# Optimization experiments

Hardware: AMD Instinct MI355X
Metric: run time of the kernel (lower is better)

Reference implementation:

```python
import jax, jax.numpy as jnp
import numpy as np

B, T, ENC, DEC, OUT = 512, 128, 256, 256, 1
Tm1 = T - 1


def setup_inputs() -> dict:
    key = jax.random.key(0)
    ks = jax.random.split(key, 14)
    s = lambda k, shape, scale=0.05: (jax.random.normal(k, shape, dtype=jnp.float32) * scale)
    return {
        "input_encoded": jax.random.normal(ks[0], (B, Tm1, ENC), dtype=jnp.float32),
        "y_history": jax.random.normal(ks[1], (B, Tm1, OUT), dtype=jnp.float32),
        # attn_layer: Linear(2*DEC+ENC -> ENC), Tanh, Linear(ENC -> 1)
        "W_attn1": s(ks[2], (ENC, 2 * DEC + ENC)),
        "b_attn1": s(ks[3], (ENC,)),
        "W_attn2": s(ks[4], (1, ENC)),
        "b_attn2": s(ks[5], (1,)),
        # single-layer LSTM cell (input_size=OUT, hidden=DEC); gate order i,f,g,o
        "W_ih": s(ks[6], (4 * DEC, OUT)),
        "W_hh": s(ks[7], (4 * DEC, DEC)),
        "b_ih": s(ks[8], (4 * DEC,)),
        "b_hh": s(ks[9], (4 * DEC,)),
        # fc: Linear(ENC+OUT -> OUT); torch code re-inits weight ~ N(0,1)
        "W_fc": jax.random.normal(ks[10], (OUT, ENC + OUT), dtype=jnp.float32),
        "b_fc": s(ks[11], (OUT,)),
        # fc_final: Linear(DEC+ENC -> OUT)
        "W_fcf": s(ks[12], (OUT, DEC + ENC)),
        "b_fcf": s(ks[13], (OUT,)),
    }


def reference(input_encoded, y_history, W_attn1, b_attn1, W_attn2, b_attn2,
              W_ih, W_hh, b_ih, b_hh, W_fc, b_fc, W_fcf, b_fcf):
    Bsz, tm1, enc = input_encoded.shape
    dec = W_hh.shape[1]
    h0 = jnp.zeros((Bsz, dec), dtype=input_encoded.dtype)
    c0 = jnp.zeros_like(h0)
    ctx0 = jnp.zeros((Bsz, enc), dtype=input_encoded.dtype)

    def step(carry, y_t):
        h, c, _ = carry  # h, c: [B, DEC]; y_t: [B, OUT]
        hs = jnp.broadcast_to(h[:, None, :], (Bsz, tm1, dec))
        cs = jnp.broadcast_to(c[:, None, :], (Bsz, tm1, dec))
        x = jnp.concatenate([hs, cs, input_encoded], axis=-1)  # [B, Tm1, 2*DEC+ENC]
        score = jnp.tanh(x @ W_attn1.T + b_attn1) @ W_attn2.T + b_attn2  # [B, Tm1, 1]
        attn = jax.nn.softmax(score[..., 0], axis=1)  # [B, Tm1]
        context = jnp.einsum('bt,bte->be', attn, input_encoded)  # [B, ENC]
        y_tilde = jnp.concatenate([context, y_t], axis=1) @ W_fc.T + b_fc  # [B, OUT]
        gates = y_tilde @ W_ih.T + b_ih + h @ W_hh.T + b_hh  # [B, 4*DEC]
        i, f, g, o = jnp.split(gates, 4, axis=1)
        c_new = jax.nn.sigmoid(f) * c + jax.nn.sigmoid(i) * jnp.tanh(g)
        h_new = jax.nn.sigmoid(o) * jnp.tanh(c_new)
        return (h_new, c_new, context), attn

    (h, c, context), attn_rows = jax.lax.scan(
        step, (h0, c0, ctx0), jnp.swapaxes(y_history, 0, 1))
    weight = jnp.swapaxes(attn_rows, 0, 1)  # [B, Tm1, Tm1]
    out = jnp.concatenate([h, context], axis=1) @ W_fcf.T + b_fcf  # [B, OUT]
    return out, weight
```

## Files before the change

kernel.cpp:

```cpp
#include <hip/hip_runtime.h>

typedef _Float16 f16;
typedef _Float16 h2 __attribute__((ext_vector_type(2)));
typedef _Float16 h4 __attribute__((ext_vector_type(4)));
typedef _Float16 h8 __attribute__((ext_vector_type(8)));

#define T127 127

__device__ __forceinline__ float rcp_f(float x) { return __builtin_amdgcn_rcpf(x); }

__device__ __forceinline__ float fdot2(h2 a, h2 b, float c) {
  return __builtin_amdgcn_fdot2(a, b, c, false);
}
__device__ __forceinline__ h2 mk2(f16 a, f16 b) { h2 v; v[0] = a; v[1] = b; return v; }

__device__ __forceinline__ float fast_tanh(float x) {
  x = fminf(fmaxf(x, -12.f), 12.f);
  float e = __expf(2.f * x);
  return (e - 1.f) * rcp_f(e + 1.f);
}
__device__ __forceinline__ float fast_sig(float x) {
  x = fminf(fmaxf(x, -30.f), 30.f);
  return rcp_f(1.f + __expf(-x));
}

__global__ void pack_wa1c(const float* __restrict__ Wa1, f16* __restrict__ wsA) {
  int tid = blockIdx.x * 256 + threadIdx.x;
  int it = tid >> 9, L = tid & 511;
  int k = L >> 1, g2 = L & 1;
  const float* src = Wa1 + (size_t)k * 768 + 256 + g2 * 128 + it * 8;
  f16* dst = wsA + (size_t)tid * 8;
#pragma unroll
  for (int j = 0; j < 8; ++j) dst[j] = (f16)src[j];
}

__global__ void pack_whh2(const float* __restrict__ Whh, f16* __restrict__ wsH) {
  int tid = blockIdx.x * 256 + threadIdx.x;
  int m = tid >> 9, L = tid & 511;
  int row = L + (m & 1) * 512;
  int it = m >> 1;
  const float* src = Whh + (size_t)row * 256 + it * 8;
  f16* dst = wsH + (size_t)tid * 8;
#pragma unroll
  for (int j = 0; j < 8; ++j) dst[j] = (f16)src[j];
}

__global__ __attribute__((amdgpu_flat_work_group_size(512, 512)))
void decoder_kernel(
    const float* __restrict__ enc,
    const float* __restrict__ yhist,
    const float* __restrict__ Wa1,
    const float* __restrict__ ba1,
    const float* __restrict__ Wa2,
    const float* __restrict__ ba2,
    const float* __restrict__ Wih,
    const float* __restrict__ bih,
    const float* __restrict__ bhh,
    const float* __restrict__ Wfc,
    const float* __restrict__ bfc,
    const float* __restrict__ Wfcf,
    const float* __restrict__ bfcf,
    const f16* __restrict__ wsA,
    const f16* __restrict__ wsH,
    float* __restrict__ outp)
{
  __shared__ __align__(16) f16 tE1[2][T127][272];
  __shared__ __align__(16) f16 hch[2][4][136];
  __shared__ __align__(16) float s_arr[2][4][68];
  __shared__ __align__(16) float score_s[2][128];
  __shared__ __align__(16) float p_s[2][128];
  __shared__ __align__(16) float q_s[2][128];
  __shared__ __align__(16) char ovl[8192];
  __shared__ __align__(16) float w2_lds[256];
  __shared__ __align__(16) float yh_s[2][128];
  __shared__ float ytil[2], ctxq_s[2], red[8];

  float* gact = (float*)ovl;
  f16* est = (f16*)ovl;

  const int L = threadIdx.x;
  const int b0 = blockIdx.x * 2;
  const int kL = L >> 1;
  const int g2 = L & 1;

  for (int i = L; i < 1088; i += 512) ((f16*)hch)[i] = (f16)0.f;
  if (L < 256) {
    w2_lds[L] = Wa2[L];
    int bb = L >> 7, tt = L & 127;
    if (tt < T127) yh_s[bb][tt] = yhist[(size_t)(b0 + bb) * T127 + tt];
  }
  float c_reg = 0.f;

  {
    h2 we1[64];
    {
      const float4* wrow = (const float4*)(Wa1 + (size_t)kL * 768 + 512 + g2 * 128);
#pragma unroll
      for (int i = 0; i < 32; ++i) {
        float4 w = wrow[i];
        we1[2 * i]     = mk2((f16)w.x, (f16)w.y);
        we1[2 * i + 1] = mk2((f16)w.z, (f16)w.w);
      }
    }
    const int prow = L >> 6;
    const int lm = L & 63;
    const int sg = lm >> 4;
    const int si = (lm * 4) & 63;

#pragma unroll 1
    for (int tt = 0; tt < 32; ++tt) {
      __syncthreads();
      {
        int bbs = prow >> 2, j4 = prow & 3, j = tt * 4 + j4;
        float4 v = make_float4(0.f, 0.f, 0.f, 0.f);
        if (j < T127)
          v = *(const float4*)(enc + (((size_t)(b0 + bbs)) * T127 + j) * 256 + lm * 4);
        h4 hv; hv[0] = (f16)v.x; hv[1] = (f16)v.y; hv[2] = (f16)v.z; hv[3] = (f16)v.w;
        *(h4*)(est + prow * 288 + sg * 72 + si) = hv;
      }
      __syncthreads();
#pragma unroll 1
      for (int P = 0; P < 8; ++P) {
        int bbs = P >> 2, j4 = P & 3, j = tt * 4 + j4;
        const h8* ep = (const h8*)(est + P * 288 + (2 * g2) * 72);
        const h8* ep2 = (const h8*)(est + P * 288 + (2 * g2 + 1) * 72);
        float a0 = 0.f, a1 = 0.f;
#pragma unroll
        for (int r = 0; r < 8; ++r) {
          h8 e8 = ep[r];
          a0 = fdot2(we1[4 * r + 0], mk2(e8[0], e8[1]), a0);
          a1 = fdot2(we1[4 * r + 1], mk2(e8[2], e8[3]), a1);
          a0 = fdot2(we1[4 * r + 2], mk2(e8[4], e8[5]), a0);
          a1 = fdot2(we1[4 * r + 3], mk2(e8[6], e8[7]), a1);
        }
#pragma unroll
        for (int r = 0; r < 8; ++r) {
          h8 e8 = ep2[r];
          a0 = fdot2(we1[32 + 4 * r + 0], mk2(e8[0], e8[1]), a0);
          a1 = fdot2(we1[32 + 4 * r + 1], mk2(e8[2], e8[3]), a1);
          a0 = fdot2(we1[32 + 4 * r + 2], mk2(e8[4], e8[5]), a0);
          a1 = fdot2(we1[32 + 4 * r + 3], mk2(e8[6], e8[7]), a1);
        }
        float acc = a0 + a1;
        acc += __shfl_xor(acc, 1, 64);
        if (g2 == 0 && j < T127)
          tE1[bbs][j][(kL >> 6) * 68 + (kL & 63)] = (f16)fast_tanh(acc);
      }
      {
        int bbs = prow >> 2, j4 = prow & 3, j = tt * 4 + j4;
        float4 wp4 = *(const float4*)(Wfc + lm * 4);
        float4 wq4 = *(const float4*)(Wfcf + 256 + lm * 4);
        h4 ev = *(const h4*)(est + prow * 288 + sg * 72 + si);
        float pacc = (float)ev[0] * wp4.x + (float)ev[1] * wp4.y + (float)ev[2] * wp4.z + (float)ev[3] * wp4.w;
        float qacc = (float)ev[0] * wq4.x + (float)ev[1] * wq4.y + (float)ev[2] * wq4.z + (float)ev[3] * wq4.w;
#pragma unroll
        for (int s = 32; s; s >>= 1) {
          pacc += __shfl_xor(pacc, s, 64);
          qacc += __shfl_xor(qacc, s, 64);
        }
        if (lm == 0 && j < T127) { p_s[bbs][j] = pacc; q_s[bbs][j] = qacc; }
      }
    }
  }
  __syncthreads();

  h2 w1h[64];
  {
    const float4* wrow = (const float4*)(Wa1 + (size_t)kL * 768 + g2 * 128);
#pragma unroll
    for (int i = 0; i < 32; ++i) {
      float4 w = wrow[i];
      w1h[2 * i]     = mk2((f16)w.x, (f16)w.y);
      w1h[2 * i + 1] = mk2((f16)w.z, (f16)w.w);
    }
  }
  const float b1k = ba1[kL];
  const float wihA = Wih[L];
  const float wihB = Wih[512 + L];
  const float biasA = bih[L] + bhh[L];
  const float biasB = bih[512 + L] + bhh[512 + L];
  const float ba2v = ba2[0];
  const float wfcy = Wfc[256];
  const float bfc0 = bfc[0];
  const int g_u = L & 3;
  __syncthreads();

#pragma unroll 1
  for (int t = 0; t < T127; ++t) {
    const h8* wA = (const h8*)wsA + L;
    const h8* wH = (const h8*)wsH + L;
    h8 a0 = wA[0], a1 = wA[512];
    h8 p0 = wH[0], p1 = wH[512], p2 = wH[1024], p3 = wH[1536];

    float u0a = 0.f, u0b = 0.f, u1a = 0.f, u1b = 0.f;
    {
      const h8* hp0 = (const h8*)&hch[0][g2][0];
      const h8* hp1 = (const h8*)&hch[1][g2][0];
#pragma unroll
      for (int r = 0; r < 16; ++r) {
        h8 x = hp0[r];
        u0a = fdot2(w1h[4 * r + 0], mk2(x[0], x[1]), u0a);
        u0b = fdot2(w1h[4 * r + 1], mk2(x[2], x[3]), u0b);
        u0a = fdot2(w1h[4 * r + 2], mk2(x[4], x[5]), u0a);
        u0b = fdot2(w1h[4 * r + 3], mk2(x[6], x[7]), u0b);
        h8 y = hp1[r];
        u1a = fdot2(w1h[4 * r + 0], mk2(y[0], y[1]), u1a);
        u1b = fdot2(w1h[4 * r + 1], mk2(y[2], y[3]), u1b);
        u1a = fdot2(w1h[4 * r + 2], mk2(y[4], y[5]), u1a);
        u1b = fdot2(w1h[4 * r + 3], mk2(y[6], y[7]), u1b);
      }
    }
    {
      const h8* cp0 = (const h8*)&hch[0][2 + g2][0];
      const h8* cp1 = (const h8*)&hch[1][2 + g2][0];
#pragma unroll 1
      for (int it = 0; it < 16; ++it) {
        h8 nxt = wA[((it + 2) & 15) * 512];
        h8 c0 = cp0[it], c1 = cp1[it];
        u0a = fdot2(mk2(a0[0], a0[1]), mk2(c0[0], c0[1]), u0a);
        u0b = fdot2(mk2(a0[2], a0[3]), mk2(c0[2], c0[3]), u0b);
        u0a = fdot2(mk2(a0[4], a0[5]), mk2(c0[4], c0[5]), u0a);
        u0b = fdot2(mk2(a0[6], a0[7]), mk2(c0[6], c0[7]), u0b);
        u1a = fdot2(mk2(a0[0], a0[1]), mk2(c1[0], c1[1]), u1a);
        u1b = fdot2(mk2(a0[2], a0[3]), mk2(c1[2], c1[3]), u1b);
        u1a = fdot2(mk2(a0[4], a0[5]), mk2(c1[4], c1[5]), u1a);
        u1b = fdot2(mk2(a0[6], a0[7]), mk2(c1[6], c1[7]), u1b);
        a0 = a1; a1 = nxt;
      }
    }

    float ghA0 = 0.f, ghA1 = 0.f, ghB0 = 0.f, ghB1 = 0.f;
#pragma unroll 1
    for (int m = 0; m < 64; m += 2) {
      h8 n0 = wH[((m + 4) & 63) * 512];
      h8 n1 = wH[((m + 5) & 63) * 512];
      int it = m >> 1;
      int ch = it >> 4, off = (it & 15) * 8;
      h8 x = *(const h8*)&hch[0][ch][off];
      h8 y = *(const h8*)&hch[1][ch][off];
      ghA0 = fdot2(mk2(p0[0], p0[1]), mk2(x[0], x[1]), ghA0);
      ghA0 = fdot2(mk2(p0[2], p0[3]), mk2(x[2], x[3]), ghA0);
      ghA0 = fdot2(mk2(p0[4], p0[5]), mk2(x[4], x[5]), ghA0);
      ghA0 = fdot2(mk2(p0[6], p0[7]), mk2(x[6], x[7]), ghA0);
      ghA1 = fdot2(mk2(p0[0], p0[1]), mk2(y[0], y[1]), ghA1);
      ghA1 = fdot2(mk2(p0[2], p0[3]), mk2(y[2], y[3]), ghA1);
      ghA1 = fdot2(mk2(p0[4], p0[5]), mk2(y[4], y[5]), ghA1);
      ghA1 = fdot2(mk2(p0[6], p0[7]), mk2(y[6], y[7]), ghA1);
      ghB0 = fdot2(mk2(p1[0], p1[1]), mk2(x[0], x[1]), ghB0);
      ghB0 = fdot2(mk2(p1[2], p1[3]), mk2(x[2], x[3]), ghB0);
      ghB0 = fdot2(mk2(p1[4], p1[5]), mk2(x[4], x[5]), ghB0);
      ghB0 = fdot2(mk2(p1[6], p1[7]), mk2(x[6], x[7]), ghB0);
      ghB1 = fdot2(mk2(p1[0], p1[1]), mk2(y[0], y[1]), ghB1);
      ghB1 = fdot2(mk2(p1[2], p1[3]), mk2(y[2], y[3]), ghB1);
      ghB1 = fdot2(mk2(p1[4], p1[5]), mk2(y[4], y[5]), ghB1);
      ghB1 = fdot2(mk2(p1[6], p1[7]), mk2(y[6], y[7]), ghB1);
      p0 = p2; p1 = p3; p2 = n0; p3 = n1;
    }

    {
      float u0 = u0a + u0b, u1 = u1a + u1b;
      u0 += __shfl_xor(u0, 1, 64);
      u1 += __shfl_xor(u1, 1, 64);
      if (g2 == 0) s_arr[0][kL >> 6][kL & 63] = fast_tanh(u0 + b1k);
      else         s_arr[1][kL >> 6][kL & 63] = fast_tanh(u1 + b1k);
    }
    __syncthreads();

#pragma unroll
    for (int half = 0; half < 2; ++half) {
      const int pr = (L >> 2) + half * 128;
      if (pr < 254) {
        const int bb = pr & 1;
        const int j = pr >> 1;
        const h4* tp = (const h4*)&tE1[bb][j][g_u * 68];
        const float4* sp = (const float4*)&s_arr[bb][g_u][0];
        const float4* w2p = (const float4*)&w2_lds[g_u * 64];
        float acc0 = 0.f, acc1 = 0.f;
#pragma unroll
        for (int i = 0; i < 16; ++i) {
          h4 tv = tp[i];
          float4 sv = sp[i];
          float4 wv = w2p[i];
          float t0 = (float)tv[0], t1 = (float)tv[1], t2 = (float)tv[2], t3 = (float)tv[3];
          acc0 = fmaf(wv.x * (sv.x + t0), rcp_f(fmaf(sv.x, t0, 1.f)), acc0);
          acc1 = fmaf(wv.y * (sv.y + t1), rcp_f(fmaf(sv.y, t1, 1.f)), acc1);
          acc0 = fmaf(wv.z * (sv.z + t2), rcp_f(fmaf(sv.z, t2, 1.f)), acc0);
          acc1 = fmaf(wv.w * (sv.w + t3), rcp_f(fmaf(sv.w, t3, 1.f)), acc1);
        }
        float acc = acc0 + acc1;
        acc += __shfl_xor(acc, 1, 64);
        acc += __shfl_xor(acc, 2, 64);
        if (g_u == 0) score_s[bb][j] = acc + ba2v;
      }
    }
    __syncthreads();

    {
      const int wv = L >> 6, ln = L & 63;
      if (wv < 2) {
        const int bb = wv;
        const int batch = b0 + bb;
        float x0 = score_s[bb][ln];
        float x1 = (ln < 63) ? score_s[bb][64 + ln] : -3.4e38f;
        float m = fmaxf(x0, x1);
#pragma unroll
        for (int s = 32; s; s >>= 1) m = fmaxf(m, __shfl_xor(m, s, 64));
        float e0 = __expf(x0 - m);
        float e1 = (ln < 63) ? __expf(x1 - m) : 0.f;
        float ssum = e0 + e1;
#pragma unroll
        for (int s = 32; s; s >>= 1) ssum += __shfl_xor(ssum, s, 64);
        float rs = rcp_f(ssum);
        float aa0 = e0 * rs, aa1 = e1 * rs;
        float* wout = outp + 512 + ((size_t)batch * T127 + t) * T127;
        wout[ln] = aa0;
        if (ln < 63) wout[64 + ln] = aa1;
        float cw = aa0 * p_s[bb][ln] + ((ln < 63) ? aa1 * p_s[bb][64 + ln] : 0.f);
#pragma unroll
        for (int s = 32; s; s >>= 1) cw += __shfl_xor(cw, s, 64);
        if (ln == 0) ytil[bb] = cw + wfcy * yh_s[bb][t] + bfc0;
        if (t == T127 - 1) {
          float cq = aa0 * q_s[bb][ln] + ((ln < 63) ? aa1 * q_s[bb][64 + ln] : 0.f);
#pragma unroll
          for (int s = 32; s; s >>= 1) cq += __shfl_xor(cq, s, 64);
          if (ln == 0) ctxq_s[bb] = cq;
        }
      }
    }
    __syncthreads();

    {
      float yt0 = ytil[0], yt1 = ytil[1];
      float gA0 = ghA0 + wihA * yt0 + biasA;
      float gA1 = ghA1 + wihA * yt1 + biasA;
      float gB0 = ghB0 + wihB * yt0 + biasB;
      float gB1 = ghB1 + wihB * yt1 + biasB;
      float aA0 = fast_sig(gA0), aA1 = fast_sig(gA1);
      bool isg = (L < 256);
      float aB0 = isg ? fast_tanh(gB0) : fast_sig(gB0);
      float aB1 = isg ? fast_tanh(gB1) : fast_sig(gB1);
      gact[0 * 1024 + L] = aA0;
      gact[1 * 1024 + L] = aA1;
      gact[0 * 1024 + 512 + L] = aB0;
      gact[1 * 1024 + 512 + L] = aB1;
    }
    __syncthreads();

    {
      const int bb = L >> 8, kk = L & 255;
      float gi = gact[bb * 1024 + kk];
      float gf = gact[bb * 1024 + 256 + kk];
      float gg = gact[bb * 1024 + 512 + kk];
      float go = gact[bb * 1024 + 768 + kk];
      float cn = gf * c_reg + gi * gg;
      float hn = go * fast_tanh(cn);
      c_reg = cn;
      hch[bb][kk >> 7][kk & 127] = (f16)hn;
      hch[bb][2 + (kk >> 7)][kk & 127] = (f16)cn;
      if (t == T127 - 1) {
        float po = Wfcf[kk] * hn;
#pragma unroll
        for (int s = 32; s; s >>= 1) po += __shfl_xor(po, s, 64);
        if ((L & 63) == 0) red[L >> 6] = po;
      }
    }
    __syncthreads();
  }

  if (L < 2) {
    float o = red[L * 4] + red[L * 4 + 1] + red[L * 4 + 2] + red[L * 4 + 3] + ctxq_s[L] + bfcf[0];
    outp[b0 + L] = o;
  }
}

extern "C" void kernel_launch(void* const* d_in, const int* in_sizes, int n_in,
                              void* d_out, int out_size, void* d_ws, size_t ws_size,
                              hipStream_t stream) {
  (void)in_sizes; (void)n_in; (void)out_size; (void)ws_size;
  f16* wsA = (f16*)d_ws;
  f16* wsH = wsA + 65536;
  pack_wa1c<<<32, 256, 0, stream>>>((const float*)d_in[2], wsA);
  pack_whh2<<<128, 256, 0, stream>>>((const float*)d_in[7], wsH);
  decoder_kernel<<<256, 512, 0, stream>>>(
      (const float*)d_in[0], (const float*)d_in[1], (const float*)d_in[2],
      (const float*)d_in[3], (const float*)d_in[4], (const float*)d_in[5],
      (const float*)d_in[6], (const float*)d_in[8], (const float*)d_in[9],
      (const float*)d_in[10], (const float*)d_in[11], (const float*)d_in[12],
      (const float*)d_in[13], wsA, wsH, (float*)d_out);
}
```

Measured before the change: 1.926 ms.

## Interleave attention score computation with hidden-gate matvec and drop barriers

Moves the tanh/s_arr write and its barrier ahead of the W_hh gate matvec, then fuses the attention score accumulation into that same loop so LDS/transcendental work overlaps the weight loads. Every wave now computes the softmax redundantly, so ytil stays in registers and two __syncthreads per step go away. The softmax max-subtraction is dropped, and the tE1 row stride is padded from 272 to 280 halfs to change LDS bank mapping. Dropping the max subtraction risks overflow in exp if scores become large, and the redundant softmax adds ALU work on every wave.

After: 1.825 ms. 1.06x faster.

```diff
diff --git a/kernel.cpp b/kernel.cpp
--- a/kernel.cpp
+++ b/kernel.cpp
@@ -64,7 +64,7 @@
     const f16* __restrict__ wsH,
     float* __restrict__ outp)
 {
-  __shared__ __align__(16) f16 tE1[2][T127][272];
+  __shared__ __align__(16) f16 tE1[2][T127][280];
   __shared__ __align__(16) f16 hch[2][4][136];
   __shared__ __align__(16) float s_arr[2][4][68];
   __shared__ __align__(16) float score_s[2][128];
@@ -73,7 +73,7 @@
   __shared__ __align__(16) char ovl[8192];
   __shared__ __align__(16) float w2_lds[256];
   __shared__ __align__(16) float yh_s[2][128];
-  __shared__ float ytil[2], ctxq_s[2], red[8];
+  __shared__ float ctxq_s[2], red[8];
 
   float* gact = (float*)ovl;
   f16* est = (f16*)ovl;
@@ -190,7 +190,7 @@
     const h8* wA = (const h8*)wsA + L;
     const h8* wH = (const h8*)wsH + L;
     h8 a0 = wA[0], a1 = wA[512];
-    h8 p0 = wH[0], p1 = wH[512], p2 = wH[1024], p3 = wH[1536];
+    h8 p0 = wH[0], p1 = wH[512];
 
     float u0a = 0.f, u0b = 0.f, u1a = 0.f, u1b = 0.f;
     {
@@ -228,14 +228,28 @@
         a0 = a1; a1 = nxt;
       }
     }
+    {
+      float u0 = u0a + u0b, u1 = u1a + u1b;
+      u0 += __shfl_xor(u0, 1, 64);
+      u1 += __shfl_xor(u1, 1, 64);
+      if (g2 == 0) s_arr[0][kL >> 6][kL & 63] = fast_tanh(u0 + b1k);
+      else         s_arr[1][kL >> 6][kL & 63] = fast_tanh(u1 + b1k);
+    }
+    __syncthreads();
 
     float ghA0 = 0.f, ghA1 = 0.f, ghB0 = 0.f, ghB1 = 0.f;
-#pragma unroll 1
-    for (int m = 0; m < 64; m += 2) {
-      h8 n0 = wH[((m + 4) & 63) * 512];
-      h8 n1 = wH[((m + 5) & 63) * 512];
-      int it = m >> 1;
-      int ch = it >> 4, off = (it & 15) * 8;
+    float acc0 = 0.f, acc1 = 0.f;
+    int pr = L >> 2;
+    int bbB = pr & 1, jB = pr >> 1;
+    const h4* tp = (const h4*)&tE1[bbB][jB][g_u * 68];
+    const float4* sp = (const float4*)&s_arr[bbB][g_u][0];
+    const float4* w2p = (const float4*)&w2_lds[g_u * 64];
+#pragma unroll 1
+    for (int i = 0; i < 32; ++i) {
+      int m = 2 * i;
+      h8 n0 = wH[((m + 2) & 63) * 512];
+      h8 n1 = wH[((m + 3) & 63) * 512];
+      int ch = i >> 4, off = (i & 15) * 8;
       h8 x = *(const h8*)&hch[0][ch][off];
       h8 y = *(const h8*)&hch[1][ch][off];
       ghA0 = fdot2(mk2(p0[0], p0[1]), mk2(x[0], x[1]), ghA0);
@@ -254,87 +268,71 @@
       ghB1 = fdot2(mk2(p1[2], p1[3]), mk2(y[2], y[3]), ghB1);
       ghB1 = fdot2(mk2(p1[4], p1[5]), mk2(y[4], y[5]), ghB1);
       ghB1 = fdot2(mk2(p1[6], p1[7]), mk2(y[6], y[7]), ghB1);
-      p0 = p2; p1 = p3; p2 = n0; p3 = n1;
-    }
-
-    {
-      float u0 = u0a + u0b, u1 = u1a + u1b;
-      u0 += __shfl_xor(u0, 1, 64);
-      u1 += __shfl_xor(u1, 1, 64);
-      if (g2 == 0) s_arr[0][kL >> 6][kL & 63] = fast_tanh(u0 + b1k);
-      else         s_arr[1][kL >> 6][kL & 63] = fast_tanh(u1 + b1k);
+      {
+        int ii = i & 15;
+        h4 tv = tp[ii];
+        float4 sv = sp[ii];
+        float4 wv = w2p[ii];
+        float t0 = (float)tv[0], t1 = (float)tv[1], t2 = (float)tv[2], t3 = (float)tv[3];
+        acc0 = fmaf(wv.x * (sv.x + t0), rcp_f(fmaf(sv.x, t0, 1.f)), acc0);
+        acc1 = fmaf(wv.y * (sv.y + t1), rcp_f(fmaf(sv.y, t1, 1.f)), acc1);
+        acc0 = fmaf(wv.z * (sv.z + t2), rcp_f(fmaf(sv.z, t2, 1.f)), acc0);
+        acc1 = fmaf(wv.w * (sv.w + t3), rcp_f(fmaf(sv.w, t3, 1.f)), acc1);
+        if (ii == 15) {
+          float acc = acc0 + acc1;
+          acc += __shfl_xor(acc, 1, 64);
+          acc += __shfl_xor(acc, 2, 64);
+          if (g_u == 0 && pr < 254) score_s[bbB][jB] = acc + ba2v;
+          acc0 = 0.f; acc1 = 0.f;
+          pr = (L >> 2) + 128;
+          int prc = (pr < 254) ? pr : 253;
+          bbB = prc & 1; jB = prc >> 1;
+          tp = (const h4*)&tE1[bbB][jB][g_u * 68];
+          sp = (const float4*)&s_arr[bbB][g_u][0];
+        }
+      }
+      p0 = n0; p1 = n1;
     }
     __syncthreads();
 
-#pragma unroll
-    for (int half = 0; half < 2; ++half) {
-      const int pr = (L >> 2) + half * 128;
-      if (pr < 254) {
-        const int bb = pr & 1;
-        const int j = pr >> 1;
-        const h4* tp = (const h4*)&tE1[bb][j][g_u * 68];
-        const float4* sp = (const float4*)&s_arr[bb][g_u][0];
-        const float4* w2p = (const float4*)&w2_lds[g_u * 64];
-        float acc0 = 0.f, acc1 = 0.f;
-#pragma unroll
-        for (int i = 0; i < 16; ++i) {
-          h4 tv = tp[i];
-          float4 sv = sp[i];
-          float4 wv = w2p[i];
-          float t0 = (float)tv[0], t1 = (float)tv[1], t2 = (float)tv[2], t3 = (float)tv[3];
-          acc0 = fmaf(wv.x * (sv.x + t0), rcp_f(fmaf(sv.x, t0, 1.f)), acc0);
-          acc1 = fmaf(wv.y * (sv.y + t1), rcp_f(fmaf(sv.y, t1, 1.f)), acc1);
-          acc0 = fmaf(wv.z * (sv.z + t2), rcp_f(fmaf(sv.z, t2, 1.f)), acc0);
-          acc1 = fmaf(wv.w * (sv.w + t3), rcp_f(fmaf(sv.w, t3, 1.f)), acc1);
-        }
-        float acc = acc0 + acc1;
-        acc += __shfl_xor(acc, 1, 64);
-        acc += __shfl_xor(acc, 2, 64);
-        if (g_u == 0) score_s[bb][j] = acc + ba2v;
-      }
-    }
-    __syncthreads();
-
-    {
-      const int wv = L >> 6, ln = L & 63;
-      if (wv < 2) {
-        const int bb = wv;
-        const int batch = b0 + bb;
+    float ytil0, ytil1;
+    {
+      const int ln = L & 63;
+      const int wv = L >> 6;
+#pragma unroll
+      for (int bb = 0; bb < 2; ++bb) {
         float x0 = score_s[bb][ln];
-        float x1 = (ln < 63) ? score_s[bb][64 + ln] : -3.4e38f;
-        float m = fmaxf(x0, x1);
-#pragma unroll
-        for (int s = 32; s; s >>= 1) m = fmaxf(m, __shfl_xor(m, s, 64));
-        float e0 = __expf(x0 - m);
-        float e1 = (ln < 63) ? __expf(x1 - m) : 0.f;
+        float e0 = __expf(x0);
+        float e1 = (ln < 63) ? __expf(score_s[bb][64 + ln]) : 0.f;
         float ssum = e0 + e1;
 #pragma unroll
         for (int s = 32; s; s >>= 1) ssum += __shfl_xor(ssum, s, 64);
         float rs = rcp_f(ssum);
         float aa0 = e0 * rs, aa1 = e1 * rs;
-        float* wout = outp + 512 + ((size_t)batch * T127 + t) * T127;
-        wout[ln] = aa0;
-        if (ln < 63) wout[64 + ln] = aa1;
+        if (wv == bb) {
+          float* wout = outp + 512 + ((size_t)(b0 + bb) * T127 + t) * T127;
+          wout[ln] = aa0;
+          if (ln < 63) wout[64 + ln] = aa1;
+        }
         float cw = aa0 * p_s[bb][ln] + ((ln < 63) ? aa1 * p_s[bb][64 + ln] : 0.f);
 #pragma unroll
         for (int s = 32; s; s >>= 1) cw += __shfl_xor(cw, s, 64);
-        if (ln == 0) ytil[bb] = cw + wfcy * yh_s[bb][t] + bfc0;
+        float yt = cw + wfcy * yh_s[bb][t] + bfc0;
+        if (bb == 0) ytil0 = yt; else ytil1 = yt;
         if (t == T127 - 1) {
           float cq = aa0 * q_s[bb][ln] + ((ln < 63) ? aa1 * q_s[bb][64 + ln] : 0.f);
 #pragma unroll
           for (int s = 32; s; s >>= 1) cq += __shfl_xor(cq, s, 64);
-          if (ln == 0) ctxq_s[bb] = cq;
-        }
-      }
-    }
-    __syncthreads();
-
-    {
-      float yt0 = ytil[0], yt1 = ytil[1];
-      float gA0 = ghA0 + wihA * yt0 + biasA;
-      float gA1 = ghA1 + wihA * yt1 + biasA;
-      float gB0 = ghB0 + wihB * yt0 + biasB;
-      float gB1 = ghB1 + wihB * yt1 + biasB;
+          if (L == 0) ctxq_s[bb] = cq;
+        }
+      }
+    }
+
+    {
+      float gA0 = ghA0 + wihA * ytil0 + biasA;
+      float gA1 = ghA1 + wihA * ytil1 + biasA;
+      float gB0 = ghB0 + wihB * ytil0 + biasB;
+      float gB1 = ghB1 + wihB * ytil1 + biasB;
       float aA0 = fast_sig(gA0), aA1 = fast_sig(gA1);
       bool isg = (L < 256);
       float aB0 = isg ? fast_tanh(gB0) : fast_sig(gB0);
```
